# Kernel tuning notes

Measured on AMD Instinct MI355X. Metric: run time of the kernel, lower is better.

## Reference

```python
import jax, jax.numpy as jnp
import numpy as np


def _generate_anchors(anc, grid):
    # anc: (A,2) = (w,h); grid: (B,H,W,2) = (x,y) centers
    # -> anchors (B,A,H,W,4) = (x_tl, y_tl, x_br, y_br)
    centers = jnp.concatenate([grid, grid], axis=-1)[:, None, :, :, :]  # (B,1,H,W,4)
    half = 0.5 * jnp.stack([-anc[:, 0], -anc[:, 1], anc[:, 0], anc[:, 1]], axis=-1)  # (A,4)
    return centers + half[None, :, None, None, :]


def _generate_proposals_yolo(anchors, offsets):
    # anchors, offsets: (B,A,H,W,4) -> proposals (B,A,H,W,4)
    x_ca = 0.5 * (anchors[..., 0] + anchors[..., 2])
    y_ca = 0.5 * (anchors[..., 1] + anchors[..., 3])
    wa = anchors[..., 2] - anchors[..., 0]
    ha = anchors[..., 3] - anchors[..., 1]
    # YOLO transform: center shift is additive, size is log-space scale
    x_cp = x_ca + offsets[..., 0]
    y_cp = y_ca + offsets[..., 1]
    wp = wa * jnp.exp(offsets[..., 2])
    hp = ha * jnp.exp(offsets[..., 3])
    return jnp.stack([x_cp - 0.5 * wp, y_cp - 0.5 * hp,
                      x_cp + 0.5 * wp, y_cp + 0.5 * hp], axis=-1)


def _iou(proposals, bboxes):
    # proposals: (B,A,H,W,4); bboxes: (B,N,5) -> iou_mat (B, A*H*W, N)
    B = proposals.shape[0]
    p = proposals.reshape(B, -1, 1, 4)          # (B, AHW, 1, 4)
    b = bboxes[:, None, :, :4]                   # (B, 1,  N, 4)
    tl = jnp.maximum(p[..., :2], b[..., :2])     # (B, AHW, N, 2)
    br = jnp.minimum(p[..., 2:], b[..., 2:])
    no_inter = (tl[..., 0] > br[..., 0]) | (tl[..., 1] > br[..., 1])
    aoi = (br[..., 0] - tl[..., 0]) * (br[..., 1] - tl[..., 1])
    aoi = jnp.where(no_inter, 0.0, aoi)
    aop = (p[..., 2] - p[..., 0]) * (p[..., 3] - p[..., 1])  # (B, AHW, 1)
    aob = (b[..., 2] - b[..., 0]) * (b[..., 3] - b[..., 1])  # (B, 1,  N)
    return aoi / (aop + aob - aoi)


def setup_inputs() -> dict:
    key = jax.random.key(0)
    k1, k2, k3, k4 = jax.random.split(key, 4)
    B, A, H, W, N = 16, 9, 56, 56, 64
    anc = jax.random.uniform(k1, (A, 2), dtype=jnp.float32)          # anchor (w,h) shapes
    grid = jax.random.uniform(k2, (B, H, W, 2), dtype=jnp.float32)   # cell centers
    offsets = jax.random.normal(k3, (B, A, H, W, 4), dtype=jnp.float32)
    bboxes = jax.random.uniform(k4, (B, N, 5), dtype=jnp.float32)    # GT boxes (x1,y1,x2,y2,cls)
    return {"anc": anc, "grid": grid, "offsets": offsets, "bboxes": bboxes}


def reference(anc, grid, offsets, bboxes):
    anchors = _generate_anchors(anc, grid)
    proposals = _generate_proposals_yolo(anchors, offsets)
    iou_mat = _iou(proposals, bboxes)
    return iou_mat
```

## Files before the change

kernel.cpp:

```cpp
#include <hip/hip_runtime.h>
#include <hip/hip_bf16.h>


constexpr int B_ = 16;
constexpr int A_ = 9;
constexpr int H_ = 56;
constexpr int W_ = 56;
constexpr int N_ = 64;
constexpr int HW_ = H_ * W_;
constexpr int P_ = A_ * HW_;
constexpr int BLOCK = 192;
constexpr int BLKS_PER_BATCH = P_ / BLOCK;

typedef float floatx4 __attribute__((ext_vector_type(4)));

__global__ __launch_bounds__(BLOCK) void ssd_iou_kernel(
    const float* __restrict__ anc,
    const float* __restrict__ grid,
    const float* __restrict__ offsets,
    const float* __restrict__ bboxes,
    float* __restrict__ out)
{
    __shared__ float4 s_box[BLOCK];

    const int t  = threadIdx.x;
    const int b  = blockIdx.x / BLKS_PER_BATCH;
    const int lb = blockIdx.x - b * BLKS_PER_BATCH;
    const int p0 = lb * BLOCK;

    {
        const int lp = p0 + t;
        const int a  = lp / HW_;
        const int hw = lp - a * HW_;
        const int gp = b * P_ + lp;

        const float4 off = reinterpret_cast<const float4*>(offsets)[gp];
        const float2 g   = reinterpret_cast<const float2*>(grid)[b * HW_ + hw];
        const float  aw  = anc[2 * a + 0];
        const float  ah  = anc[2 * a + 1];

        const float xc = g.x + off.x;
        const float yc = g.y + off.y;
        const float wp = aw * __expf(off.z);
        const float hp = ah * __expf(off.w);

        float4 box;
        box.x = xc - 0.5f * wp;
        box.y = yc - 0.5f * hp;
        box.z = xc + 0.5f * wp;
        box.w = yc + 0.5f * hp;
        s_box[t] = box;
    }
    __syncthreads();

    const int wave = t >> 6;
    const int lane = t & 63;
    const int q    = lane >> 4;
    const int g    = lane & 15;

    float bx0[4], by0[4], bx1[4], by1[4], aob[4];
    #pragma unroll
    for (int k = 0; k < 4; ++k) {
        const float* bb = bboxes + ((size_t)(b * N_ + 4 * g + k)) * 5;
        bx0[k] = bb[0];
        by0[k] = bb[1];
        bx1[k] = bb[2];
        by1[k] = bb[3];
        aob[k] = (bx1[k] - bx0[k]) * (by1[k] - by0[k]);
    }

    const int pbase = wave * 64;
    float* obase = out + ((size_t)(b * P_ + p0 + pbase + q)) * N_ + 4 * g;

    #pragma unroll
    for (int j = 0; j < 16; ++j) {
        const float4 pr = s_box[pbase + 4 * j + q];
        const float aop = (pr.z - pr.x) * (pr.w - pr.y);

        floatx4 res;
        #pragma unroll
        for (int k = 0; k < 4; ++k) {
            const float tlx = fmaxf(pr.x, bx0[k]);
            const float tly = fmaxf(pr.y, by0[k]);
            const float brx = fminf(pr.z, bx1[k]);
            const float bry = fminf(pr.w, by1[k]);

            const float iw  = fmaxf(brx - tlx, 0.0f);
            const float ih  = fmaxf(bry - tly, 0.0f);
            const float aoi = iw * ih;

            const float denom = aop + aob[k] - aoi;
            res[k] = aoi * __builtin_amdgcn_rcpf(denom);
        }

        *reinterpret_cast<floatx4*>(obase + (size_t)(4 * j) * N_) = res;
    }
}

extern "C" void kernel_launch(void* const* d_in, const int* in_sizes, int n_in,
                              void* d_out, int out_size, void* d_ws, size_t ws_size,
                              hipStream_t stream) {
    const float* anc     = (const float*)d_in[0];
    const float* grid    = (const float*)d_in[1];
    const float* offsets = (const float*)d_in[2];
    const float* bboxes  = (const float*)d_in[3];
    float* out = (float*)d_out;

    const int nblocks = B_ * BLKS_PER_BATCH;
    ssd_iou_kernel<<<nblocks, BLOCK, 0, stream>>>(anc, grid, offsets, bboxes, out);
}
```

Before: 130.8 us.

## Process three proposal chunks per block with double-buffered prefetch

```diff
diff --git a/kernel.cpp b/kernel.cpp
--- a/kernel.cpp
+++ b/kernel.cpp
@@ -10,7 +10,8 @@
 constexpr int HW_ = H_ * W_;
 constexpr int P_ = A_ * HW_;
 constexpr int BLOCK = 192;
-constexpr int BLKS_PER_BATCH = P_ / BLOCK;
+constexpr int CPB = 3;
+constexpr int BLKS_PER_BATCH = P_ / (BLOCK * CPB);
 
 typedef float floatx4 __attribute__((ext_vector_type(4)));
 
@@ -21,47 +22,44 @@
     const float* __restrict__ bboxes,
     float* __restrict__ out)
 {
-    __shared__ float4 s_box[BLOCK];
+    __shared__ float4 s_box[2][BLOCK];
 
-    const int t  = threadIdx.x;
-    const int b  = blockIdx.x / BLKS_PER_BATCH;
-    const int lb = blockIdx.x - b * BLKS_PER_BATCH;
-    const int p0 = lb * BLOCK;
+    const int t   = threadIdx.x;
+    const int b   = blockIdx.x / BLKS_PER_BATCH;
+    const int blk = blockIdx.x - b * BLKS_PER_BATCH;
+    const int lp0 = blk * (BLOCK * CPB);
 
-    {
-        const int lp = p0 + t;
+    auto fetch = [&](int lp, float4& off, float2& g, float& aw, float& ah) {
         const int a  = lp / HW_;
         const int hw = lp - a * HW_;
-        const int gp = b * P_ + lp;
-
-        const float4 off = reinterpret_cast<const float4*>(offsets)[gp];
-        const float2 g   = reinterpret_cast<const float2*>(grid)[b * HW_ + hw];
-        const float  aw  = anc[2 * a + 0];
-        const float  ah  = anc[2 * a + 1];
-
+        off = reinterpret_cast<const float4*>(offsets)[b * P_ + lp];
+        g   = reinterpret_cast<const float2*>(grid)[b * HW_ + hw];
+        aw  = anc[2 * a + 0];
+        ah  = anc[2 * a + 1];
+    };
+    auto decode = [&](int buf, const float4& off, const float2& g,
+                      float aw, float ah) {
         const float xc = g.x + off.x;
         const float yc = g.y + off.y;
         const float wp = aw * __expf(off.z);
         const float hp = ah * __expf(off.w);
-
         float4 box;
         box.x = xc - 0.5f * wp;
         box.y = yc - 0.5f * hp;
         box.z = xc + 0.5f * wp;
         box.w = yc + 0.5f * hp;
-        s_box[t] = box;
-    }
-    __syncthreads();
+        s_box[buf][t] = box;
+    };
 
     const int wave = t >> 6;
     const int lane = t & 63;
     const int q    = lane >> 4;
-    const int g    = lane & 15;
+    const int g16  = lane & 15;
 
     float bx0[4], by0[4], bx1[4], by1[4], aob[4];
     #pragma unroll
     for (int k = 0; k < 4; ++k) {
-        const float* bb = bboxes + ((size_t)(b * N_ + 4 * g + k)) * 5;
+        const float* bb = bboxes + ((size_t)(b * N_ + 4 * g16 + k)) * 5;
         bx0[k] = bb[0];
         by0[k] = bb[1];
         bx1[k] = bb[2];
@@ -69,31 +67,47 @@
         aob[k] = (bx1[k] - bx0[k]) * (by1[k] - by0[k]);
     }
 
-    const int pbase = wave * 64;
-    float* obase = out + ((size_t)(b * P_ + p0 + pbase + q)) * N_ + 4 * g;
+    float4 off; float2 g; float aw, ah;
+    fetch(lp0 + t, off, g, aw, ah);
+    decode(0, off, g, aw, ah);
+    __syncthreads();
 
-    #pragma unroll
-    for (int j = 0; j < 16; ++j) {
-        const float4 pr = s_box[pbase + 4 * j + q];
-        const float aop = (pr.z - pr.x) * (pr.w - pr.y);
+    for (int c = 0; c < CPB; ++c) {
+        if (c + 1 < CPB)
+            fetch(lp0 + (c + 1) * BLOCK + t, off, g, aw, ah);
 
-        floatx4 res;
+        const float4* sb = &s_box[c & 1][wave * 64];
+        float* obase = out
+            + ((size_t)(b * P_ + lp0 + c * BLOCK + wave * 64 + q)) * N_
+            + 4 * g16;
+
         #pragma unroll
-        for (int k = 0; k < 4; ++k) {
-            const float tlx = fmaxf(pr.x, bx0[k]);
-            const float tly = fmaxf(pr.y, by0[k]);
-            const float brx = fminf(pr.z, bx1[k]);
-            const float bry = fminf(pr.w, by1[k]);
+        for (int j = 0; j < 16; ++j) {
+            const float4 pr = sb[4 * j + q];
+            const float aop = (pr.z - pr.x) * (pr.w - pr.y);
 
-            const float iw  = fmaxf(brx - tlx, 0.0f);
-            const float ih  = fmaxf(bry - tly, 0.0f);
-            const float aoi = iw * ih;
+            floatx4 res;
+            #pragma unroll
+            for (int k = 0; k < 4; ++k) {
+                const float tlx = fmaxf(pr.x, bx0[k]);
+                const float tly = fmaxf(pr.y, by0[k]);
+                const float brx = fminf(pr.z, bx1[k]);
+                const float bry = fminf(pr.w, by1[k]);
 
-            const float denom = aop + aob[k] - aoi;
-            res[k] = aoi * __builtin_amdgcn_rcpf(denom);
+                const float iw  = fmaxf(brx - tlx, 0.0f);
+                const float ih  = fmaxf(bry - tly, 0.0f);
+                const float aoi = iw * ih;
+
+                const float denom = aop + aob[k] - aoi;
+                res[k] = aoi * __builtin_amdgcn_rcpf(denom);
+            }
+
+            *reinterpret_cast<floatx4*>(obase + (size_t)(4 * j) * N_) = res;
         }
 
-        *reinterpret_cast<floatx4*>(obase + (size_t)(4 * j) * N_) = res;
+        if (c + 1 < CPB)
+            decode((c + 1) & 1, off, g, aw, ah);
+        __syncthreads();
     }
 }
 
```

After: 135.2 us. 1.03x slower.
